# Kernel optimization log

Hardware: AMD Instinct MI355X
Metric: run time of the kernel (lower is better)

## Reference

```python
import jax, jax.numpy as jnp
import numpy as np

B, IN, OUT, HS, NBDA = 128, 256, 256, 512, 1

def setup_inputs() -> dict:
    key = jax.random.key(0)
    ks = jax.random.split(key, 16)
    d = {}
    d["inputs"] = jax.random.normal(ks[0], (B, IN), dtype=jnp.float32)
    d["hidden"] = jax.random.normal(ks[1], (B, HS), dtype=jnp.float32)
    d["hebb"] = jax.random.normal(ks[2], (B, HS, HS), dtype=jnp.float32) * 0.1
    # learned params (torch.nn.Linear: y = x @ W.T + b)
    d["i2h_w"] = jax.random.normal(ks[3], (HS, IN), dtype=jnp.float32) * (1.0 / np.sqrt(IN))
    d["i2h_b"] = jnp.zeros((HS,), dtype=jnp.float32)
    d["w"] = 0.01 * jax.random.uniform(ks[4], (HS, HS), dtype=jnp.float32)
    d["alpha"] = 0.01 * jax.random.uniform(ks[5], (HS, HS), dtype=jnp.float32)
    d["h2o_w"] = jax.random.normal(ks[6], (OUT, HS), dtype=jnp.float32) * (1.0 / np.sqrt(HS))
    d["h2o_b"] = jnp.zeros((OUT,), dtype=jnp.float32)
    d["h2v_w"] = jax.random.normal(ks[7], (1, HS), dtype=jnp.float32) * (1.0 / np.sqrt(HS))
    d["h2v_b"] = jnp.zeros((1,), dtype=jnp.float32)
    d["h2da_w"] = jax.random.normal(ks[8], (NBDA, HS), dtype=jnp.float32) * (1.0 / np.sqrt(HS))
    d["h2da_b"] = jnp.zeros((NBDA,), dtype=jnp.float32)
    return d

def reference(inputs, hidden, hebb, i2h_w, i2h_b, w, alpha, h2o_w, h2o_b,
              h2v_w, h2v_b, h2da_w, h2da_b):
    # hactiv = tanh(i2h(x) + (w + alpha*hebb) @ hidden), per-sample weight matrix
    pre = inputs @ i2h_w.T + i2h_b                              # [B, HS]
    w_eff = w + alpha * hebb                                    # [B, HS, HS]
    rec = jnp.einsum('bij,bj->bi', w_eff, hidden)               # [B, HS]
    hactiv = jnp.tanh(pre + rec)                                # [B, HS]
    activout = hactiv @ h2o_w.T + h2o_b                         # [B, OUT]
    valueout = hactiv @ h2v_w.T + h2v_b                         # [B, 1]
    da = jnp.tanh(hactiv @ h2da_w.T + h2da_b)                   # [B, NBDA]
    # outer-product Hebbian update, DA-modulated, clamped to [-1, 1]
    deltahebb = hactiv[:, :, None] * hidden[:, None, :]         # [B, HS, HS]
    hebb_new = jnp.clip(hebb + da[:, :1, None] * deltahebb, -1.0, 1.0)
    return activout, valueout, hactiv, hebb_new
```

## Files before the change

kernel.cpp:

```cpp
#include <hip/hip_runtime.h>
#include <cstddef>

#define B_    128
#define IN_   256
#define OUT_  256
#define HS_   512

__global__ __launch_bounds__(256) void k1_hactiv(
    const float* __restrict__ inputs,
    const float* __restrict__ hidden,
    const float* __restrict__ hebb,
    const float* __restrict__ i2h_w,
    const float* __restrict__ i2h_b,
    const float* __restrict__ w,
    const float* __restrict__ alpha,
    float* __restrict__ hactiv)
{
    const int b     = blockIdx.x & (B_ - 1);
    const int chunk = blockIdx.x >> 7;
    const int tid   = threadIdx.x;
    const int wave  = tid >> 6;
    const int lane  = tid & 63;

    const float4* hid4 = (const float4*)(hidden + (size_t)b * HS_);
    const float4  h0   = hid4[lane];
    const float4  h1   = hid4[lane + 64];
    const float4  in4  = ((const float4*)(inputs + (size_t)b * IN_))[lane];

    const int i0 = chunk * 64 + wave * 16;

    for (int r = 0; r < 16; ++r) {
        const int i = i0 + r;
        const float4* hb = (const float4*)(hebb + ((size_t)b * HS_ + i) * HS_);
        const float4* wr = (const float4*)(w     + (size_t)i * HS_);
        const float4* ar = (const float4*)(alpha + (size_t)i * HS_);

        const float4 hb0 = hb[lane];
        const float4 hb1 = hb[lane + 64];
        const float4 wv0 = wr[lane];
        const float4 wv1 = wr[lane + 64];
        const float4 av0 = ar[lane];
        const float4 av1 = ar[lane + 64];
        const float4 iw  = ((const float4*)(i2h_w + (size_t)i * IN_))[lane];

        float acc;
        acc  = (wv0.x + av0.x * hb0.x) * h0.x;
        acc += (wv0.y + av0.y * hb0.y) * h0.y;
        acc += (wv0.z + av0.z * hb0.z) * h0.z;
        acc += (wv0.w + av0.w * hb0.w) * h0.w;
        acc += (wv1.x + av1.x * hb1.x) * h1.x;
        acc += (wv1.y + av1.y * hb1.y) * h1.y;
        acc += (wv1.z + av1.z * hb1.z) * h1.z;
        acc += (wv1.w + av1.w * hb1.w) * h1.w;
        acc += iw.x * in4.x + iw.y * in4.y + iw.z * in4.z + iw.w * in4.w;

        #pragma unroll
        for (int off = 32; off > 0; off >>= 1)
            acc += __shfl_down(acc, off, 64);

        if (lane == 0)
            hactiv[(size_t)b * HS_ + i] = tanhf(acc + i2h_b[i]);
    }
}

__global__ __launch_bounds__(256) void k2_heads(
    const float* __restrict__ hactiv,
    const float* __restrict__ h2o_w,
    const float* __restrict__ h2o_b,
    const float* __restrict__ h2v_w,
    const float* __restrict__ h2v_b,
    const float* __restrict__ h2da_w,
    const float* __restrict__ h2da_b,
    float* __restrict__ activout,
    float* __restrict__ valueout,
    float* __restrict__ da)
{
    const int b   = blockIdx.x;
    const int tid = threadIdx.x;

    __shared__ float s_h[HS_];
    __shared__ float red_v[256];
    __shared__ float red_d[256];

    for (int t = tid; t < HS_; t += 256)
        s_h[t] = hactiv[(size_t)b * HS_ + t];
    __syncthreads();

    const float4* wr  = (const float4*)(h2o_w + (size_t)tid * HS_);
    const float4* sh4 = (const float4*)s_h;
    float acc = 0.f;
    #pragma unroll 4
    for (int q = 0; q < HS_ / 4; ++q) {
        const float4 wv = wr[q];
        const float4 hv = sh4[q];
        acc += wv.x * hv.x + wv.y * hv.y + wv.z * hv.z + wv.w * hv.w;
    }
    activout[(size_t)b * OUT_ + tid] = acc + h2o_b[tid];

    float pv = 0.f, pd = 0.f;
    for (int t = tid; t < HS_; t += 256) {
        const float hv = s_h[t];
        pv += hv * h2v_w[t];
        pd += hv * h2da_w[t];
    }
    red_v[tid] = pv;
    red_d[tid] = pd;
    __syncthreads();
    for (int s = 128; s > 0; s >>= 1) {
        if (tid < s) {
            red_v[tid] += red_v[tid + s];
            red_d[tid] += red_d[tid + s];
        }
        __syncthreads();
    }
    if (tid == 0) {
        valueout[b] = red_v[0] + h2v_b[0];
        da[b]       = tanhf(red_d[0] + h2da_b[0]);
    }
}

__global__ __launch_bounds__(256) void k3_hebb(
    const float* __restrict__ hebb,
    const float* __restrict__ hidden,
    const float* __restrict__ hactiv,
    const float* __restrict__ da,
    float* __restrict__ hebb_new)
{
    const int tid = threadIdx.x;
    const size_t base = (size_t)blockIdx.x * 1024;

    #pragma unroll
    for (int k = 0; k < 4; ++k) {
        const size_t idx = base + (size_t)k * 256 + tid;
        const int j4  = (int)(idx & 127);
        const int row = (int)(idx >> 7);
        const int i   = row & (HS_ - 1);
        const int b   = row >> 9;

        const float scale = da[b] * hactiv[(size_t)b * HS_ + i];
        const float4 hv = ((const float4*)hebb)[idx];
        const float4 hd = ((const float4*)hidden)[(size_t)b * (HS_ / 4) + j4];

        float4 r;
        r.x = fminf(fmaxf(fmaf(scale, hd.x, hv.x), -1.f), 1.f);
        r.y = fminf(fmaxf(fmaf(scale, hd.y, hv.y), -1.f), 1.f);
        r.z = fminf(fmaxf(fmaf(scale, hd.z, hv.z), -1.f), 1.f);
        r.w = fminf(fmaxf(fmaf(scale, hd.w, hv.w), -1.f), 1.f);
        ((float4*)hebb_new)[idx] = r;
    }
}

extern "C" void kernel_launch(void* const* d_in, const int* in_sizes, int n_in,
                              void* d_out, int out_size, void* d_ws, size_t ws_size,
                              hipStream_t stream)
{
    const float* inputs = (const float*)d_in[0];
    const float* hidden = (const float*)d_in[1];
    const float* hebb   = (const float*)d_in[2];
    const float* i2h_w  = (const float*)d_in[3];
    const float* i2h_b  = (const float*)d_in[4];
    const float* w      = (const float*)d_in[5];
    const float* alpha  = (const float*)d_in[6];
    const float* h2o_w  = (const float*)d_in[7];
    const float* h2o_b  = (const float*)d_in[8];
    const float* h2v_w  = (const float*)d_in[9];
    const float* h2v_b  = (const float*)d_in[10];
    const float* h2da_w = (const float*)d_in[11];
    const float* h2da_b = (const float*)d_in[12];

    float* out = (float*)d_out;
    float* activout = out;
    float* valueout = out + 32768;
    float* hactiv   = out + 32768 + 128;
    float* hebb_new = out + 32768 + 128 + 65536;

    float* da = (float*)d_ws;

    k1_hactiv<<<dim3(1024), dim3(256), 0, stream>>>(
        inputs, hidden, hebb, i2h_w, i2h_b, w, alpha, hactiv);

    k2_heads<<<dim3(B_), dim3(256), 0, stream>>>(
        hactiv, h2o_w, h2o_b, h2v_w, h2v_b, h2da_w, h2da_b,
        activout, valueout, da);

    k3_hebb<<<dim3(8192), dim3(256), 0, stream>>>(
        hebb, hidden, hactiv, da, hebb_new);
}
```

Baseline: 300.9 us.

## Fuse recurrence, heads and Hebbian update into one cooperative persistent kernel

```diff
diff --git a/kernel.cpp b/kernel.cpp
--- a/kernel.cpp
+++ b/kernel.cpp
@@ -1,12 +1,23 @@
 #include <hip/hip_runtime.h>
+#include <hip/hip_cooperative_groups.h>
 #include <cstddef>
+
+namespace cg = cooperative_groups;
 
 #define B_    128
 #define IN_   256
 #define OUT_  256
 #define HS_   512
 
-__global__ __launch_bounds__(256) void k1_hactiv(
+#define NBLK_  256
+#define NTHR_  512
+#define ROUNDS_ 4
+
+__device__ __forceinline__ float clip1(float x) {
+    return fminf(fmaxf(x, -1.f), 1.f);
+}
+
+__global__ __launch_bounds__(NTHR_, 2) void fused_plastic(
     const float* __restrict__ inputs,
     const float* __restrict__ hidden,
     const float* __restrict__ hebb,
@@ -14,7 +25,168 @@
     const float* __restrict__ i2h_b,
     const float* __restrict__ w,
     const float* __restrict__ alpha,
-    float* __restrict__ hactiv)
+    const float* __restrict__ h2o_w,
+    const float* __restrict__ h2o_b,
+    const float* __restrict__ h2v_w,
+    const float* __restrict__ h2v_b,
+    const float* __restrict__ h2da_w,
+    const float* __restrict__ h2da_b,
+    float* __restrict__ activout,
+    float* __restrict__ valueout,
+    float* __restrict__ hactiv,
+    float* __restrict__ hebb_new,
+    float* __restrict__ ws_pd,
+    float* __restrict__ ws_pv)
+{
+    cg::grid_group grid = cg::this_grid();
+
+    const int blk  = blockIdx.x;
+    const int xcd  = blk & 7;
+    const int slot = blk >> 3;
+    const int sub  = slot >> 3;
+    const int bs   = slot & 7;
+    const int tid  = threadIdx.x;
+    const int wave = tid >> 6;
+    const int lane = tid & 63;
+
+    __shared__ float s_pd[8];
+    __shared__ float s_pv[8];
+    __shared__ float s_h[HS_];
+    __shared__ float s_part[128 * 4];
+
+    for (int r = 0; r < ROUNDS_; ++r) {
+        const int b = r * 32 + xcd * 4 + sub;
+
+        const float4* hid4 = (const float4*)(hidden + (size_t)b * HS_);
+        const float4 h0  = hid4[lane];
+        const float4 h1  = hid4[lane + 64];
+        const float4 in4 = ((const float4*)(inputs + (size_t)b * IN_))[lane];
+
+        const int i_base = bs * 64 + wave * 8;
+
+        float hb_s[8][8];
+        float h_row[8];
+        float pd = 0.f, pv = 0.f;
+
+        #pragma unroll
+        for (int q = 0; q < 8; ++q) {
+            const int i = i_base + q;
+            const float4* hbp = (const float4*)(hebb + ((size_t)b * HS_ + i) * HS_);
+            const float4 hb0 = hbp[lane];
+            const float4 hb1 = hbp[lane + 64];
+            const float4* wr = (const float4*)(w     + (size_t)i * HS_);
+            const float4* ar = (const float4*)(alpha + (size_t)i * HS_);
+            const float4 wv0 = wr[lane], wv1 = wr[lane + 64];
+            const float4 av0 = ar[lane], av1 = ar[lane + 64];
+            const float4 iw  = ((const float4*)(i2h_w + (size_t)i * IN_))[lane];
+
+            float acc;
+            acc  = (wv0.x + av0.x * hb0.x) * h0.x;
+            acc += (wv0.y + av0.y * hb0.y) * h0.y;
+            acc += (wv0.z + av0.z * hb0.z) * h0.z;
+            acc += (wv0.w + av0.w * hb0.w) * h0.w;
+            acc += (wv1.x + av1.x * hb1.x) * h1.x;
+            acc += (wv1.y + av1.y * hb1.y) * h1.y;
+            acc += (wv1.z + av1.z * hb1.z) * h1.z;
+            acc += (wv1.w + av1.w * hb1.w) * h1.w;
+            acc += iw.x * in4.x + iw.y * in4.y + iw.z * in4.z + iw.w * in4.w;
+
+            #pragma unroll
+            for (int off = 1; off < 64; off <<= 1)
+                acc += __shfl_xor(acc, off, 64);
+
+            const float h = tanhf(acc + i2h_b[i]);
+            h_row[q] = h;
+
+            hb_s[q][0] = hb0.x; hb_s[q][1] = hb0.y; hb_s[q][2] = hb0.z; hb_s[q][3] = hb0.w;
+            hb_s[q][4] = hb1.x; hb_s[q][5] = hb1.y; hb_s[q][6] = hb1.z; hb_s[q][7] = hb1.w;
+
+            if (lane == 0) {
+                hactiv[(size_t)b * HS_ + i] = h;
+                pd += h * h2da_w[i];
+                pv += h * h2v_w[i];
+            }
+        }
+
+        if (lane == 0) { s_pd[wave] = pd; s_pv[wave] = pv; }
+        __syncthreads();
+        if (tid == 0) {
+            float sd = 0.f, sv = 0.f;
+            #pragma unroll
+            for (int k = 0; k < 8; ++k) { sd += s_pd[k]; sv += s_pv[k]; }
+            ws_pd[b * 8 + bs] = sd;
+            ws_pv[b * 8 + bs] = sv;
+        }
+        __threadfence();
+        grid.sync();
+
+        float sd = 0.f, sv = 0.f;
+        #pragma unroll
+        for (int k = 0; k < 8; ++k) {
+            sd += ws_pd[b * 8 + k];
+            sv += ws_pv[b * 8 + k];
+        }
+        const float da_b = tanhf(sd + h2da_b[0]);
+        if (bs == 0 && tid == 0)
+            valueout[b] = sv + h2v_b[0];
+
+        #pragma unroll
+        for (int q = 0; q < 8; ++q) {
+            const int i = i_base + q;
+            const float sc = da_b * h_row[q];
+            float4 o0, o1;
+            o0.x = clip1(fmaf(sc, h0.x, hb_s[q][0]));
+            o0.y = clip1(fmaf(sc, h0.y, hb_s[q][1]));
+            o0.z = clip1(fmaf(sc, h0.z, hb_s[q][2]));
+            o0.w = clip1(fmaf(sc, h0.w, hb_s[q][3]));
+            o1.x = clip1(fmaf(sc, h1.x, hb_s[q][4]));
+            o1.y = clip1(fmaf(sc, h1.y, hb_s[q][5]));
+            o1.z = clip1(fmaf(sc, h1.z, hb_s[q][6]));
+            o1.w = clip1(fmaf(sc, h1.w, hb_s[q][7]));
+            float4* op = (float4*)(hebb_new + ((size_t)b * HS_ + i) * HS_);
+            op[lane]      = o0;
+            op[lane + 64] = o1;
+        }
+    }
+
+    const int k16 = slot >> 1;
+    const int ha  = slot & 1;
+    const int ba  = (k16 >> 2) * 32 + xcd * 4 + (k16 & 3);
+
+    __syncthreads();
+    if (tid < 128)
+        ((float4*)s_h)[tid] = ((const float4*)(hactiv + (size_t)ba * HS_))[tid];
+    __syncthreads();
+
+    {
+        const int oo = tid & 127;
+        const int qq = tid >> 7;
+        const int o  = ha * 128 + oo;
+        const float4* wp = (const float4*)(h2o_w + (size_t)o * HS_);
+        const float4* hp = (const float4*)s_h;
+        float acc = 0.f;
+        #pragma unroll 8
+        for (int c = 0; c < 32; ++c) {
+            const float4 wv = wp[qq * 32 + c];
+            const float4 hv = hp[qq * 32 + c];
+            acc += wv.x * hv.x + wv.y * hv.y + wv.z * hv.z + wv.w * hv.w;
+        }
+        s_part[qq * 128 + oo] = acc;
+    }
+    __syncthreads();
+    if (tid < 128) {
+        const int o = ha * 128 + tid;
+        activout[(size_t)ba * OUT_ + o] =
+            s_part[tid] + s_part[128 + tid] + s_part[256 + tid] + s_part[384 + tid]
+            + h2o_b[o];
+    }
+}
+
+__global__ __launch_bounds__(256) void k1_hactiv(
+    const float* __restrict__ inputs, const float* __restrict__ hidden,
+    const float* __restrict__ hebb, const float* __restrict__ i2h_w,
+    const float* __restrict__ i2h_b, const float* __restrict__ w,
+    const float* __restrict__ alpha, float* __restrict__ hactiv)
 {
     const int b     = blockIdx.x & (B_ - 1);
     const int chunk = blockIdx.x >> 7;
@@ -64,16 +236,11 @@
 }
 
 __global__ __launch_bounds__(256) void k2_heads(
-    const float* __restrict__ hactiv,
-    const float* __restrict__ h2o_w,
-    const float* __restrict__ h2o_b,
-    const float* __restrict__ h2v_w,
-    const float* __restrict__ h2v_b,
-    const float* __restrict__ h2da_w,
-    const float* __restrict__ h2da_b,
-    float* __restrict__ activout,
-    float* __restrict__ valueout,
-    float* __restrict__ da)
+    const float* __restrict__ hactiv, const float* __restrict__ h2o_w,
+    const float* __restrict__ h2o_b, const float* __restrict__ h2v_w,
+    const float* __restrict__ h2v_b, const float* __restrict__ h2da_w,
+    const float* __restrict__ h2da_b, float* __restrict__ activout,
+    float* __restrict__ valueout, float* __restrict__ da)
 {
     const int b   = blockIdx.x;
     const int tid = threadIdx.x;
@@ -120,10 +287,8 @@
 }
 
 __global__ __launch_bounds__(256) void k3_hebb(
-    const float* __restrict__ hebb,
-    const float* __restrict__ hidden,
-    const float* __restrict__ hactiv,
-    const float* __restrict__ da,
+    const float* __restrict__ hebb, const float* __restrict__ hidden,
+    const float* __restrict__ hactiv, const float* __restrict__ da,
     float* __restrict__ hebb_new)
 {
     const int tid = threadIdx.x;
@@ -174,15 +339,27 @@
     float* hactiv   = out + 32768 + 128;
     float* hebb_new = out + 32768 + 128 + 65536;
 
-    float* da = (float*)d_ws;
-
-    k1_hactiv<<<dim3(1024), dim3(256), 0, stream>>>(
-        inputs, hidden, hebb, i2h_w, i2h_b, w, alpha, hactiv);
-
-    k2_heads<<<dim3(B_), dim3(256), 0, stream>>>(
-        hactiv, h2o_w, h2o_b, h2v_w, h2v_b, h2da_w, h2da_b,
-        activout, valueout, da);
-
-    k3_hebb<<<dim3(8192), dim3(256), 0, stream>>>(
-        hebb, hidden, hactiv, da, hebb_new);
-}
+    if (ws_size >= (size_t)(2 * B_ * 8 * sizeof(float))) {
+        float* ws_pd = (float*)d_ws;
+        float* ws_pv = ws_pd + B_ * 8;
+
+        void* args[] = {
+            (void*)&inputs, (void*)&hidden, (void*)&hebb, (void*)&i2h_w,
+            (void*)&i2h_b,  (void*)&w,      (void*)&alpha, (void*)&h2o_w,
+            (void*)&h2o_b,  (void*)&h2v_w,  (void*)&h2v_b, (void*)&h2da_w,
+            (void*)&h2da_b, (void*)&activout, (void*)&valueout,
+            (void*)&hactiv, (void*)&hebb_new, (void*)&ws_pd, (void*)&ws_pv
+        };
+        hipLaunchCooperativeKernel((const void*)fused_plastic,
+                                   dim3(NBLK_), dim3(NTHR_), args, 0, stream);
+    } else {
+        float* da = (float*)d_ws;
+        k1_hactiv<<<dim3(1024), dim3(256), 0, stream>>>(
+            inputs, hidden, hebb, i2h_w, i2h_b, w, alpha, hactiv);
+        k2_heads<<<dim3(B_), dim3(256), 0, stream>>>(
+            hactiv, h2o_w, h2o_b, h2v_w, h2v_b, h2da_w, h2da_b,
+            activout, valueout, da);
+        k3_hebb<<<dim3(8192), dim3(256), 0, stream>>>(
+            hebb, hidden, hactiv, da, hebb_new);
+    }
+}
```

Measured after the change: 664.6 us. 121% more time.

## Fuse hactiv, heads and Hebbian update into one kernel with inter-block gating

Applied to the files above, without the earlier changes.

```diff
diff --git a/kernel.cpp b/kernel.cpp
--- a/kernel.cpp
+++ b/kernel.cpp
@@ -1,12 +1,21 @@
 #include <hip/hip_runtime.h>
 #include <cstddef>
+#include <cstdint>
 
 #define B_    128
 #define IN_   256
 #define OUT_  256
 #define HS_   512
 
-__global__ __launch_bounds__(256) void k1_hactiv(
+#define NTHR_  512
+#define NBLK_  512
+#define SPLIT_ 4
+
+__device__ __forceinline__ float clip1(float x) {
+    return fminf(fmaxf(x, -1.f), 1.f);
+}
+
+__global__ __launch_bounds__(NTHR_, 2) void fused_stream(
     const float* __restrict__ inputs,
     const float* __restrict__ hidden,
     const float* __restrict__ hebb,
@@ -14,7 +23,199 @@
     const float* __restrict__ i2h_b,
     const float* __restrict__ w,
     const float* __restrict__ alpha,
-    float* __restrict__ hactiv)
+    const float* __restrict__ h2o_w,
+    const float* __restrict__ h2o_b,
+    const float* __restrict__ h2v_w,
+    const float* __restrict__ h2v_b,
+    const float* __restrict__ h2da_w,
+    const float* __restrict__ h2da_b,
+    float* __restrict__ activout,
+    float* __restrict__ valueout,
+    float* __restrict__ hactiv,
+    float* __restrict__ hebb_new,
+    float* __restrict__ ws_pd,
+    float* __restrict__ ws_pv,
+    int*   __restrict__ ws_cnt)
+{
+    const int blk  = blockIdx.x;
+    const int xcd  = blk & 7;
+    const int g    = blk >> 3;
+    const int q16  = g >> 2;
+    const int s    = g & 3;
+    const int b    = xcd * 16 + q16;
+    const int tid  = threadIdx.x;
+    const int wave = tid >> 6;
+    const int lane = tid & 63;
+    const int r0   = s * 128 + wave * 16;
+    const int lr0  = wave * 16;
+
+    __shared__ float s_hrow[128];
+    __shared__ float s_pd[8], s_pv[8];
+    __shared__ float s_bc[2];
+    __shared__ float s_h[HS_];
+    __shared__ float s_part[256];
+
+    const float4* hid4 = (const float4*)(hidden + (size_t)b * HS_);
+    const float4 h0  = hid4[lane];
+    const float4 h1  = hid4[lane + 64];
+    const float4 in4 = ((const float4*)(inputs + (size_t)b * IN_))[lane];
+
+    const float4* hb4 = (const float4*)hebb + ((size_t)b * HS_) * (HS_ / 4);
+    const float4* w4  = (const float4*)w;
+    const float4* a4  = (const float4*)alpha;
+    const float4* iw4 = (const float4*)i2h_w;
+
+    float pd = 0.f, pv = 0.f;
+    for (int t = 0; t < 16; t += 2) {
+        const int i = r0 + t;
+        const float4* hpA = hb4 + (size_t)i * (HS_ / 4);
+        const float4* hpB = hpA + (HS_ / 4);
+        const float4* wpA = w4  + (size_t)i * (HS_ / 4);
+        const float4* apA = a4  + (size_t)i * (HS_ / 4);
+        const float4* ipA = iw4 + (size_t)i * (IN_ / 4);
+
+        const float4 xA0 = hpA[lane],            xA1 = hpA[lane + 64];
+        const float4 xB0 = hpB[lane],            xB1 = hpB[lane + 64];
+        const float4 wA0 = wpA[lane],            wA1 = wpA[lane + 64];
+        const float4 wB0 = wpA[128 + lane],      wB1 = wpA[128 + lane + 64];
+        const float4 aA0 = apA[lane],            aA1 = apA[lane + 64];
+        const float4 aB0 = apA[128 + lane],      aB1 = apA[128 + lane + 64];
+        const float4 iA  = ipA[lane];
+        const float4 iB  = ipA[64 + lane];
+
+        float a, c;
+        a  = (wA0.x + aA0.x * xA0.x) * h0.x;
+        a += (wA0.y + aA0.y * xA0.y) * h0.y;
+        a += (wA0.z + aA0.z * xA0.z) * h0.z;
+        a += (wA0.w + aA0.w * xA0.w) * h0.w;
+        a += (wA1.x + aA1.x * xA1.x) * h1.x;
+        a += (wA1.y + aA1.y * xA1.y) * h1.y;
+        a += (wA1.z + aA1.z * xA1.z) * h1.z;
+        a += (wA1.w + aA1.w * xA1.w) * h1.w;
+        a += iA.x * in4.x + iA.y * in4.y + iA.z * in4.z + iA.w * in4.w;
+
+        c  = (wB0.x + aB0.x * xB0.x) * h0.x;
+        c += (wB0.y + aB0.y * xB0.y) * h0.y;
+        c += (wB0.z + aB0.z * xB0.z) * h0.z;
+        c += (wB0.w + aB0.w * xB0.w) * h0.w;
+        c += (wB1.x + aB1.x * xB1.x) * h1.x;
+        c += (wB1.y + aB1.y * xB1.y) * h1.y;
+        c += (wB1.z + aB1.z * xB1.z) * h1.z;
+        c += (wB1.w + aB1.w * xB1.w) * h1.w;
+        c += iB.x * in4.x + iB.y * in4.y + iB.z * in4.z + iB.w * in4.w;
+
+        #pragma unroll
+        for (int off = 1; off < 64; off <<= 1) {
+            a += __shfl_xor(a, off, 64);
+            c += __shfl_xor(c, off, 64);
+        }
+
+        const float hA = tanhf(a + i2h_b[i]);
+        const float hB = tanhf(c + i2h_b[i + 1]);
+        if (lane == 0) {
+            s_hrow[lr0 + t]     = hA;
+            s_hrow[lr0 + t + 1] = hB;
+            float2* hp = (float2*)(hactiv + (size_t)b * HS_ + i);
+            *hp = make_float2(hA, hB);
+            pd += hA * h2da_w[i] + hB * h2da_w[i + 1];
+            pv += hA * h2v_w[i]  + hB * h2v_w[i + 1];
+        }
+    }
+
+    if (lane == 0) { s_pd[wave] = pd; s_pv[wave] = pv; }
+    __syncthreads();
+
+    if (tid == 0) {
+        float sd = 0.f, sv = 0.f;
+        #pragma unroll
+        for (int k = 0; k < 8; ++k) { sd += s_pd[k]; sv += s_pv[k]; }
+        __hip_atomic_fetch_add(&ws_pd[b], sd, __ATOMIC_RELAXED,
+                               __HIP_MEMORY_SCOPE_AGENT);
+        __hip_atomic_fetch_add(&ws_pv[b], sv, __ATOMIC_RELAXED,
+                               __HIP_MEMORY_SCOPE_AGENT);
+        __hip_atomic_fetch_add(&ws_cnt[b], 1, __ATOMIC_RELEASE,
+                               __HIP_MEMORY_SCOPE_AGENT);
+        while (__hip_atomic_load(&ws_cnt[b], __ATOMIC_ACQUIRE,
+                                 __HIP_MEMORY_SCOPE_AGENT) < SPLIT_)
+            __builtin_amdgcn_s_sleep(1);
+        const float pdt = __hip_atomic_load(&ws_pd[b], __ATOMIC_RELAXED,
+                                            __HIP_MEMORY_SCOPE_AGENT);
+        const float pvt = __hip_atomic_load(&ws_pv[b], __ATOMIC_RELAXED,
+                                            __HIP_MEMORY_SCOPE_AGENT);
+        s_bc[0] = tanhf(pdt + h2da_b[0]);
+        s_bc[1] = pvt + h2v_b[0];
+    }
+    __syncthreads();
+    const float da_b = s_bc[0];
+    if (s == 0 && tid == 0)
+        valueout[b] = s_bc[1];
+
+    for (int t = 0; t < 16; t += 2) {
+        const int i = r0 + t;
+        const float4* xp = hb4 + (size_t)i * (HS_ / 4);
+        const float4 x0 = xp[lane],       x1 = xp[lane + 64];
+        const float4 y0 = xp[128 + lane], y1 = xp[128 + lane + 64];
+        const float scA = da_b * s_hrow[lr0 + t];
+        const float scB = da_b * s_hrow[lr0 + t + 1];
+
+        float4 o0, o1, p0, p1;
+        o0.x = clip1(fmaf(scA, h0.x, x0.x));
+        o0.y = clip1(fmaf(scA, h0.y, x0.y));
+        o0.z = clip1(fmaf(scA, h0.z, x0.z));
+        o0.w = clip1(fmaf(scA, h0.w, x0.w));
+        o1.x = clip1(fmaf(scA, h1.x, x1.x));
+        o1.y = clip1(fmaf(scA, h1.y, x1.y));
+        o1.z = clip1(fmaf(scA, h1.z, x1.z));
+        o1.w = clip1(fmaf(scA, h1.w, x1.w));
+        p0.x = clip1(fmaf(scB, h0.x, y0.x));
+        p0.y = clip1(fmaf(scB, h0.y, y0.y));
+        p0.z = clip1(fmaf(scB, h0.z, y0.z));
+        p0.w = clip1(fmaf(scB, h0.w, y0.w));
+        p1.x = clip1(fmaf(scB, h1.x, y1.x));
+        p1.y = clip1(fmaf(scB, h1.y, y1.y));
+        p1.z = clip1(fmaf(scB, h1.z, y1.z));
+        p1.w = clip1(fmaf(scB, h1.w, y1.w));
+
+        float4* dp = (float4*)hebb_new + ((size_t)b * HS_ + i) * (HS_ / 4);
+        dp[lane]            = o0;
+        dp[lane + 64]       = o1;
+        dp[128 + lane]      = p0;
+        dp[128 + lane + 64] = p1;
+    }
+
+    if (tid < 128)
+        ((float4*)s_h)[tid] = ((const float4*)(hactiv + (size_t)b * HS_))[tid];
+    __syncthreads();
+
+    if (tid < 256) {
+        const int ol = tid & 63;
+        const int qq = tid >> 6;
+        const int o  = s * 64 + ol;
+        const float4* wp  = (const float4*)(h2o_w + (size_t)o * HS_);
+        const float4* hp4 = (const float4*)s_h;
+        float acc = 0.f;
+        #pragma unroll
+        for (int c2 = 0; c2 < 32; ++c2) {
+            const float4 wv = wp[qq * 32 + c2];
+            const float4 hv = hp4[qq * 32 + c2];
+            acc += wv.x * hv.x + wv.y * hv.y + wv.z * hv.z + wv.w * hv.w;
+        }
+        s_part[qq * 64 + ol] = acc;
+    }
+    __syncthreads();
+    if (tid < 64) {
+        const int o = s * 64 + tid;
+        activout[(size_t)b * OUT_ + o] =
+            s_part[tid] + s_part[64 + tid] + s_part[128 + tid] +
+            s_part[192 + tid] + h2o_b[o];
+    }
+}
+
+__global__ __launch_bounds__(256) void k1_hactiv(
+    const float* __restrict__ inputs, const float* __restrict__ hidden,
+    const float* __restrict__ hebb, const float* __restrict__ i2h_w,
+    const float* __restrict__ i2h_b, const float* __restrict__ w,
+    const float* __restrict__ alpha, float* __restrict__ hactiv)
 {
     const int b     = blockIdx.x & (B_ - 1);
     const int chunk = blockIdx.x >> 7;
@@ -64,16 +265,11 @@
 }
 
 __global__ __launch_bounds__(256) void k2_heads(
-    const float* __restrict__ hactiv,
-    const float* __restrict__ h2o_w,
-    const float* __restrict__ h2o_b,
-    const float* __restrict__ h2v_w,
-    const float* __restrict__ h2v_b,
-    const float* __restrict__ h2da_w,
-    const float* __restrict__ h2da_b,
-    float* __restrict__ activout,
-    float* __restrict__ valueout,
-    float* __restrict__ da)
+    const float* __restrict__ hactiv, const float* __restrict__ h2o_w,
+    const float* __restrict__ h2o_b, const float* __restrict__ h2v_w,
+    const float* __restrict__ h2v_b, const float* __restrict__ h2da_w,
+    const float* __restrict__ h2da_b, float* __restrict__ activout,
+    float* __restrict__ valueout, float* __restrict__ da)
 {
     const int b   = blockIdx.x;
     const int tid = threadIdx.x;
@@ -106,10 +302,10 @@
     red_v[tid] = pv;
     red_d[tid] = pd;
     __syncthreads();
-    for (int s = 128; s > 0; s >>= 1) {
-        if (tid < s) {
-            red_v[tid] += red_v[tid + s];
-            red_d[tid] += red_d[tid + s];
+    for (int s2 = 128; s2 > 0; s2 >>= 1) {
+        if (tid < s2) {
+            red_v[tid] += red_v[tid + s2];
+            red_d[tid] += red_d[tid + s2];
         }
         __syncthreads();
     }
@@ -120,10 +316,8 @@
 }
 
 __global__ __launch_bounds__(256) void k3_hebb(
-    const float* __restrict__ hebb,
-    const float* __restrict__ hidden,
-    const float* __restrict__ hactiv,
-    const float* __restrict__ da,
+    const float* __restrict__ hebb, const float* __restrict__ hidden,
+    const float* __restrict__ hactiv, const float* __restrict__ da,
     float* __restrict__ hebb_new)
 {
     const int tid = threadIdx.x;
@@ -174,15 +368,28 @@
     float* hactiv   = out + 32768 + 128;
     float* hebb_new = out + 32768 + 128 + 65536;
 
-    float* da = (float*)d_ws;
-
-    k1_hactiv<<<dim3(1024), dim3(256), 0, stream>>>(
-        inputs, hidden, hebb, i2h_w, i2h_b, w, alpha, hactiv);
-
-    k2_heads<<<dim3(B_), dim3(256), 0, stream>>>(
-        hactiv, h2o_w, h2o_b, h2v_w, h2v_b, h2da_w, h2da_b,
-        activout, valueout, da);
-
-    k3_hebb<<<dim3(8192), dim3(256), 0, stream>>>(
-        hebb, hidden, hactiv, da, hebb_new);
-}
+    const size_t gate_bytes = (size_t)(3 * B_) * sizeof(float);
+
+    if (ws_size >= gate_bytes) {
+        float* ws_pd  = (float*)d_ws;
+        float* ws_pv  = ws_pd + B_;
+        int*   ws_cnt = (int*)(ws_pv + B_);
+
+        hipMemsetAsync(d_ws, 0, gate_bytes, stream);
+
+        fused_stream<<<dim3(NBLK_), dim3(NTHR_), 0, stream>>>(
+            inputs, hidden, hebb, i2h_w, i2h_b, w, alpha,
+            h2o_w, h2o_b, h2v_w, h2v_b, h2da_w, h2da_b,
+            activout, valueout, hactiv, hebb_new,
+            ws_pd, ws_pv, ws_cnt);
+    } else {
+        float* da = (float*)d_ws;
+        k1_hactiv<<<dim3(1024), dim3(256), 0, stream>>>(
+            inputs, hidden, hebb, i2h_w, i2h_b, w, alpha, hactiv);
+        k2_heads<<<dim3(B_), dim3(256), 0, stream>>>(
+            hactiv, h2o_w, h2o_b, h2v_w, h2v_b, h2da_w, h2da_b,
+            activout, valueout, da);
+        k3_hebb<<<dim3(8192), dim3(256), 0, stream>>>(
+            hebb, hidden, hactiv, da, hebb_new);
+    }
+}
```

After: 327.4 us. 8.8% more time.
